# Kernel optimization log

Measured on AMD Instinct MI355X. Metric: run time of the kernel, lower is better.

Reference implementation:

```python
import jax, jax.numpy as jnp
import numpy as np

D_MODEL = 1024
N_HEADS = 16


def setup_inputs() -> dict:
    key = jax.random.key(0)
    ks = jax.random.split(key, 5)
    sigma = (1.0 / D_MODEL) ** 0.5
    return {
        "x": jax.random.normal(ks[0], (4, 2048, D_MODEL), dtype=jnp.float32),
        "W_q": jax.random.normal(ks[1], (D_MODEL, D_MODEL), dtype=jnp.float32) * sigma,
        "W_k": jax.random.normal(ks[2], (D_MODEL, D_MODEL), dtype=jnp.float32) * sigma,
        "W_v": jax.random.normal(ks[3], (D_MODEL, D_MODEL), dtype=jnp.float32) * sigma,
        "W_o": jax.random.normal(ks[4], (D_MODEL, D_MODEL), dtype=jnp.float32) * sigma,
    }


def reference(x, W_q, W_k, W_v, W_o):
    b, s, d = x.shape
    h = N_HEADS
    d_h = d // h
    # Projections: original does einsum('d_out dim, ... dim -> ... d_out') == x @ W.T
    def proj(W):
        y = jnp.einsum('bsd,ed->bse', x, W)
        # ... seq (head d_h) -> ... head seq d_h
        return y.reshape(b, s, h, d_h).transpose(0, 2, 1, 3)
    Q, K, V = proj(W_q), proj(W_k), proj(W_v)
    scale = 1.0 / jnp.sqrt(jnp.asarray(d_h, dtype=x.dtype))
    scores = jnp.einsum('bhqd,bhkd->bhqk', Q, K) * scale  # [b,h,s,s]
    causal = jnp.tril(jnp.ones((s, s), dtype=bool))
    scores = jnp.where(causal, scores, -jnp.inf)
    attn = jax.nn.softmax(scores, axis=-1)
    out = jnp.einsum('bhqk,bhkd->bhqd', attn, V)  # [b,h,s,d_h]
    out = out.transpose(0, 2, 1, 3).reshape(b, s, d)
    # einsum(Temp, W_o, '... dim1, dim dim1 -> ... dim') == Temp @ W_o.T
    return jnp.einsum('bse,de->bsd', out, W_o)
```

## Files before the change

kernel.cpp:

```cpp
#include <hip/hip_runtime.h>

typedef __attribute__((ext_vector_type(8))) short s16x8;
typedef __attribute__((ext_vector_type(4))) float f32x4;
typedef unsigned short u16;
typedef unsigned int u32;
typedef unsigned long long u64;

__device__ __forceinline__ u16 f2bf(float f) {
  unsigned u = __builtin_bit_cast(unsigned, f);
  return (u16)((u + 0x7fffu + ((u >> 16) & 1u)) >> 16);
}

#define QSCALE 0.18033688011112042f
#define MFIX 16.0f

__device__ __forceinline__ void gld16(const u16* g, u16* l) {
  __builtin_amdgcn_global_load_lds(
      (const __attribute__((address_space(1))) void*)g,
      (__attribute__((address_space(3))) void*)l, 16, 0, 0);
}

__device__ __forceinline__ u32 pack_trunc(float a, float b) {
  return __builtin_amdgcn_perm(__builtin_bit_cast(u32, b),
                               __builtin_bit_cast(u32, a), 0x07060302u);
}

__global__ __launch_bounds__(256)
void cvt_bf16(const float* __restrict__ src, u16* __restrict__ dst, int n8)
{
  const int i = blockIdx.x * 256 + threadIdx.x;
  if (i < n8) {
    f32x4 a = ((const f32x4*)src)[2 * i];
    f32x4 b = ((const f32x4*)src)[2 * i + 1];
    s16x8 pk;
    pk[0] = (short)f2bf(a[0]); pk[1] = (short)f2bf(a[1]);
    pk[2] = (short)f2bf(a[2]); pk[3] = (short)f2bf(a[3]);
    pk[4] = (short)f2bf(b[0]); pk[5] = (short)f2bf(b[1]);
    pk[6] = (short)f2bf(b[2]); pk[7] = (short)f2bf(b[3]);
    ((s16x8*)dst)[i] = pk;
  }
}

__global__ __launch_bounds__(256)
void cvt_bf16_w(const float* __restrict__ s0, const float* __restrict__ s1,
                const float* __restrict__ s2, const float* __restrict__ s3,
                u16* __restrict__ d0, u16* __restrict__ d1,
                u16* __restrict__ d2, u16* __restrict__ d3)
{
  const int ws = blockIdx.y;
  const float* src = (ws == 0) ? s0 : (ws == 1) ? s1 : (ws == 2) ? s2 : s3;
  u16* dst = (ws == 0) ? d0 : (ws == 1) ? d1 : (ws == 2) ? d2 : d3;
  const int i = blockIdx.x * 256 + threadIdx.x;
  f32x4 a = ((const f32x4*)src)[2 * i];
  f32x4 b = ((const f32x4*)src)[2 * i + 1];
  s16x8 pk;
  pk[0] = (short)f2bf(a[0]); pk[1] = (short)f2bf(a[1]);
  pk[2] = (short)f2bf(a[2]); pk[3] = (short)f2bf(a[3]);
  pk[4] = (short)f2bf(b[0]); pk[5] = (short)f2bf(b[1]);
  pk[6] = (short)f2bf(b[2]); pk[7] = (short)f2bf(b[3]);
  ((s16x8*)dst)[i] = pk;
}

__global__ __launch_bounds__(512)
void gemmQKV(const u16* __restrict__ A,
             const u16* __restrict__ B0, const u16* __restrict__ B1,
             const u16* __restrict__ B2,
             u16* __restrict__ o0, u16* __restrict__ o1, u16* __restrict__ o2)
{
  const int by = blockIdx.x;
  const int bx = blockIdx.y;
  const int bz = bx >> 2;
  const u16* Bw = (bz == 0) ? B0 : ((bz == 1) ? B1 : B2);
  u16* oQ = (bz == 0) ? o0 : ((bz == 1) ? o1 : o2);

  __shared__ u16 As[2][256 * 64];
  __shared__ u16 Bs[2][256 * 64];

  const int tid  = threadIdx.x;
  const int wid  = tid >> 6;
  const int lane = tid & 63;
  const int quad = lane >> 4;
  const int l15  = lane & 15;
  const int wr   = wid >> 2;
  const int wc   = wid & 3;

  const int srow = tid >> 3;
  const int scol = ((tid & 7) ^ (srow & 7)) * 8;
  const int wb8  = wid * 8;
  const u16* Ag = A  + (size_t)(by * 256) * 1024;
  const u16* Bg = Bw + (size_t)((bx & 3) * 256) * 1024;

#define STAGE(bf, kt)                                                          \
  do {                                                                         \
    _Pragma("unroll")                                                          \
    for (int c = 0; c < 4; ++c) {                                              \
      gld16(Ag + (size_t)(c * 64 + srow) * 1024 + (kt) * 64 + scol,            \
            &As[bf][(c * 64 + wb8) * 64]);                                     \
      gld16(Bg + (size_t)(c * 64 + srow) * 1024 + (kt) * 64 + scol,            \
            &Bs[bf][(c * 64 + wb8) * 64]);                                     \
    }                                                                          \
  } while (0)

  f32x4 acc[8][4];
  #pragma unroll
  for (int i = 0; i < 8; ++i)
    #pragma unroll
    for (int j = 0; j < 4; ++j)
      acc[i][j] = (f32x4){0.f, 0.f, 0.f, 0.f};

  const int swz = (l15 & 7) * 8;
  const int ca0 = (quad * 8) ^ swz;
  const int ca1 = (32 + quad * 8) ^ swz;

  STAGE(0, 0);
  STAGE(1, 1);
  asm volatile("s_waitcnt vmcnt(8)" ::: "memory");
  __builtin_amdgcn_s_barrier();
  __builtin_amdgcn_sched_barrier(0);

  for (int kt = 0; kt < 16; ++kt) {
    const int bf = kt & 1;
    const u16* Ab = &As[bf][(wr * 128) * 64];
    const u16* Bb = &Bs[bf][(wc * 64) * 64];
    __builtin_amdgcn_s_setprio(1);
    #pragma unroll
    for (int kh = 0; kh < 2; ++kh) {
      const int cc = kh ? ca1 : ca0;
      s16x8 bfr[4];
      #pragma unroll
      for (int nt = 0; nt < 4; ++nt)
        bfr[nt] = *(const s16x8*)&Bb[(nt * 16 + l15) * 64 + cc];
      #pragma unroll
      for (int mt = 0; mt < 8; ++mt) {
        s16x8 af = *(const s16x8*)&Ab[(mt * 16 + l15) * 64 + cc];
        #pragma unroll
        for (int nt = 0; nt < 4; ++nt)
          acc[mt][nt] = __builtin_amdgcn_mfma_f32_16x16x32_bf16(
              af, bfr[nt], acc[mt][nt], 0, 0, 0);
      }
    }
    __builtin_amdgcn_s_setprio(0);
    if (kt == 15) break;
    asm volatile("s_waitcnt lgkmcnt(0)" ::: "memory");
    __builtin_amdgcn_sched_barrier(0);
    __builtin_amdgcn_s_barrier();
    if (kt < 14) {
      STAGE(bf, kt + 2);
      asm volatile("s_waitcnt vmcnt(8)" ::: "memory");
    } else {
      asm volatile("s_waitcnt vmcnt(0)" ::: "memory");
    }
    __builtin_amdgcn_sched_barrier(0);
    __builtin_amdgcn_s_barrier();
    __builtin_amdgcn_sched_barrier(0);
  }

  #pragma unroll
  for (int mt = 0; mt < 8; ++mt)
    #pragma unroll
    for (int nt = 0; nt < 4; ++nt)
      #pragma unroll
      for (int r = 0; r < 4; ++r) {
        const int row = by * 256 + wr * 128 + mt * 16 + quad * 4 + r;
        const int col = (bx & 3) * 256 + wc * 64 + nt * 16 + l15;
        float v = acc[mt][nt][r];
        if (bz == 0) v *= QSCALE;
        const int b = row >> 11, s = row & 2047, hh = col >> 6, d = col & 63;
        oQ[(size_t)(b * 16 + hh) * 131072 + s * 64 + d] = f2bf(v);
      }
#undef STAGE
}

__global__ __launch_bounds__(256)
void gemm97o(const u16* __restrict__ A, const u16* __restrict__ B,
             float* __restrict__ oF)
{
  const int by = blockIdx.x;
  const int bx = blockIdx.y;

  __shared__ u16 As[128 * 32];
  __shared__ u16 Bs[128 * 32];

  const int tid  = threadIdx.x;
  const int w    = tid >> 6;
  const int lane = tid & 63;
  const int quad = lane >> 4;
  const int l15  = lane & 15;
  const int wm   = (w >> 1) * 64;
  const int wn   = (w & 1) * 64;

  const int arb  = w * 32;
  const int srow = lane >> 2;
  const int scol = (lane & 3) * 8;
  const u16* ga = A + (size_t)(by * 128 + arb + srow) * 1024 + scol;
  const u16* gb = B + (size_t)(bx * 128 + arb + srow) * 1024 + scol;
  u16* la0 = &As[arb * 32];
  u16* la1 = &As[(arb + 16) * 32];
  u16* lb0 = &Bs[arb * 32];
  u16* lb1 = &Bs[(arb + 16) * 32];

  f32x4 acc[4][4];
  #pragma unroll
  for (int i = 0; i < 4; ++i)
    #pragma unroll
    for (int j = 0; j < 4; ++j)
      acc[i][j] = (f32x4){0.f, 0.f, 0.f, 0.f};

  for (int k0 = 0; k0 < 1024; k0 += 32) {
    gld16(ga + k0,               la0);
    gld16(ga + k0 + 16 * 1024,   la1);
    gld16(gb + k0,               lb0);
    gld16(gb + k0 + 16 * 1024,   lb1);
    __syncthreads();

    s16x8 af[4], bf[4];
    #pragma unroll
    for (int i = 0; i < 4; ++i)
      af[i] = *(const s16x8*)&As[(wm + i * 16 + l15) * 32 + quad * 8];
    #pragma unroll
    for (int i = 0; i < 4; ++i)
      bf[i] = *(const s16x8*)&Bs[(wn + i * 16 + l15) * 32 + quad * 8];
    #pragma unroll
    for (int mt = 0; mt < 4; ++mt)
      #pragma unroll
      for (int nt = 0; nt < 4; ++nt)
        acc[mt][nt] = __builtin_amdgcn_mfma_f32_16x16x32_bf16(
            af[mt], bf[nt], acc[mt][nt], 0, 0, 0);
    __syncthreads();
  }

  #pragma unroll
  for (int mt = 0; mt < 4; ++mt)
    #pragma unroll
    for (int nt = 0; nt < 4; ++nt)
      #pragma unroll
      for (int r = 0; r < 4; ++r) {
        const int row = by * 128 + wm + mt * 16 + quad * 4 + r;
        const int col = bx * 128 + wn + nt * 16 + l15;
        oF[(size_t)row * 1024 + col] = acc[mt][nt][r];
      }
}

__global__ __launch_bounds__(256)
void vtrans(const u16* __restrict__ Vb, u16* __restrict__ VT)
{
  const int st = blockIdx.x;
  const int bh = blockIdx.y;
  __shared__ u16 T[64 * 72];
  const int tid = threadIdx.x;
  const size_t base = (size_t)bh * 131072;
  #pragma unroll
  for (int p = 0; p < 2; ++p) {
    const int idx = tid + p * 256;
    const int row = idx >> 3;
    const int col = (idx & 7) * 8;
    s16x8 v = *(const s16x8*)(Vb + base + (size_t)(st * 64 + row) * 64 + col);
    #pragma unroll
    for (int e = 0; e < 8; ++e) T[(col + e) * 72 + row] = v[e];
  }
  __syncthreads();
  #pragma unroll
  for (int p = 0; p < 2; ++p) {
    const int idx = tid + p * 256;
    const int drow = idx >> 3;
    const int scol = (idx & 7) * 8;
    *(s16x8*)(VT + base + (size_t)drow * 2048 + st * 64 + scol) =
        *(const s16x8*)&T[drow * 72 + scol];
  }
}

#define LOADKV(jj)                                                             \
  do {                                                                         \
    _Pragma("unroll")                                                          \
    for (int p = 0; p < 2; ++p) {                                              \
      const int idx = tid + p * 256;                                           \
      const int key = idx >> 3, col = (idx & 7) * 8;                           \
      kreg[p] = *(const s16x8*)(Kg + base + (size_t)((jj) * 64 + key) * 64 + col); \
    }                                                                          \
    _Pragma("unroll")                                                          \
    for (int p = 0; p < 2; ++p) {                                              \
      const int idx = tid + p * 256;                                           \
      const int d = idx >> 3, col = (idx & 7) * 8;                             \
      vreg[p] = *(const s16x8*)(VTg + base + (size_t)d * 2048 + (jj) * 64 + col); \
    }                                                                          \
  } while (0)

#define STOREKV()                                                              \
  do {                                                                         \
    _Pragma("unroll")                                                          \
    for (int p = 0; p < 2; ++p) {                                              \
      const int idx = tid + p * 256;                                           \
      const int key = idx >> 3, col = (idx & 7) * 8;                           \
      const int slot = (key & 3) * 16 + (key >> 2);                            \
      *(s16x8*)&Ks[slot * 72 + col] = kreg[p];                                 \
    }                                                                          \
    _Pragma("unroll")                                                          \
    for (int p = 0; p < 2; ++p) {                                              \
      const int idx = tid + p * 256;                                           \
      const int d = idx >> 3, col = (idx & 7) * 8;                             \
      *(s16x8*)&Vt[d * 72 + col] = vreg[p];                                    \
    }                                                                          \
  } while (0)

__global__ __launch_bounds__(256, 5)
void attn_kernel(const u16* __restrict__ Qg, const u16* __restrict__ Kg,
                 const u16* __restrict__ VTg, u16* __restrict__ out)
{
  const int bh = blockIdx.x;
  const int qt = 31 - blockIdx.y;
  const int b = bh >> 4, h = bh & 15;

  __shared__ u16 Ks[64 * 72];
  __shared__ u16 Vt[64 * 72];
  __shared__ u16 Ps[64 * 72];

  const int tid = threadIdx.x;
  const int w = tid >> 6, lane = tid & 63, quad = lane >> 4, l15 = lane & 15;
  const size_t base = (size_t)bh * 131072;

  s16x8 aq[2];
  #pragma unroll
  for (int ks = 0; ks < 2; ++ks)
    aq[ks] = *(const s16x8*)(Qg + base +
        (size_t)(qt * 64 + w * 16 + l15) * 64 + ks * 32 + quad * 8);

  u16* Pw = &Ps[(w * 16) * 72];

  s16x8 ones;
  #pragma unroll
  for (int e = 0; e < 8; ++e) ones[e] = (short)0x3F80;

  f32x4 O[4], liacc;
  #pragma unroll
  for (int dt = 0; dt < 4; ++dt) O[dt] = (f32x4){0.f, 0.f, 0.f, 0.f};
  liacc = (f32x4){0.f, 0.f, 0.f, 0.f};

  s16x8 kreg[2], vreg[2];
  LOADKV(0);
  STOREKV();
  __syncthreads();

  for (int j = 0; j <= qt; ++j) {
    if (j < qt) LOADKV(j + 1);

    f32x4 S[4];
    __builtin_amdgcn_s_setprio(1);
    #pragma unroll
    for (int nt = 0; nt < 4; ++nt) {
      s16x8 b0 = *(const s16x8*)&Ks[(nt * 16 + l15) * 72 + quad * 8];
      s16x8 b1 = *(const s16x8*)&Ks[(nt * 16 + l15) * 72 + 32 + quad * 8];
      f32x4 z = (f32x4){-MFIX, -MFIX, -MFIX, -MFIX};
      z = __builtin_amdgcn_mfma_f32_16x16x32_bf16(aq[0], b0, z, 0, 0, 0);
      z = __builtin_amdgcn_mfma_f32_16x16x32_bf16(aq[1], b1, z, 0, 0, 0);
      S[nt] = z;
    }
    __builtin_amdgcn_s_setprio(0);

    if (j == qt) {
      #pragma unroll
      for (int nt = 0; nt < 4; ++nt)
        #pragma unroll
        for (int r = 0; r < 4; ++r) {
          const int kg = 4 * l15 + nt;
          const int qg = w * 16 + quad * 4 + r;
          if (kg > qg) S[nt][r] = -1e30f;
        }
    }

    #pragma unroll
    for (int r = 0; r < 4; ++r) {
      const float p0 = __builtin_amdgcn_exp2f(S[0][r]);
      const float p1 = __builtin_amdgcn_exp2f(S[1][r]);
      const float p2 = __builtin_amdgcn_exp2f(S[2][r]);
      const float p3 = __builtin_amdgcn_exp2f(S[3][r]);
      const u64 pk = (u64)pack_trunc(p0, p1) |
                     ((u64)pack_trunc(p2, p3) << 32);
      *(u64*)&Pw[(quad * 4 + r) * 72 + 4 * l15] = pk;
    }
    s16x8 a0 = *(const s16x8*)&Pw[l15 * 72 + quad * 8];
    s16x8 a1 = *(const s16x8*)&Pw[l15 * 72 + 32 + quad * 8];

    __builtin_amdgcn_s_setprio(1);
    liacc = __builtin_amdgcn_mfma_f32_16x16x32_bf16(a0, ones, liacc, 0, 0, 0);
    liacc = __builtin_amdgcn_mfma_f32_16x16x32_bf16(a1, ones, liacc, 0, 0, 0);
    #pragma unroll
    for (int dt = 0; dt < 4; ++dt) {
      s16x8 b0 = *(const s16x8*)&Vt[(dt * 16 + l15) * 72 + quad * 8];
      s16x8 b1 = *(const s16x8*)&Vt[(dt * 16 + l15) * 72 + 32 + quad * 8];
      O[dt] = __builtin_amdgcn_mfma_f32_16x16x32_bf16(a0, b0, O[dt], 0, 0, 0);
      O[dt] = __builtin_amdgcn_mfma_f32_16x16x32_bf16(a1, b1, O[dt], 0, 0, 0);
    }
    __builtin_amdgcn_s_setprio(0);

    __syncthreads();
    if (j < qt) {
      STOREKV();
      __syncthreads();
    }
  }

  #pragma unroll
  for (int r = 0; r < 4; ++r) {
    const float inv = __builtin_amdgcn_rcpf(liacc[r]);
    const int sq = qt * 64 + w * 16 + quad * 4 + r;
    #pragma unroll
    for (int dt = 0; dt < 4; ++dt)
      out[(size_t)(b * 2048 + sq) * 1024 + h * 64 + dt * 16 + l15] =
          f2bf(O[dt][r] * inv);
  }
}

extern "C" void kernel_launch(void* const* d_in, const int* in_sizes, int n_in,
                              void* d_out, int out_size, void* d_ws, size_t ws_size,
                              hipStream_t stream) {
  (void)in_sizes; (void)n_in; (void)out_size; (void)ws_size;
  const float* x  = (const float*)d_in[0];
  const float* Wq = (const float*)d_in[1];
  const float* Wk = (const float*)d_in[2];
  const float* Wv = (const float*)d_in[3];
  const float* Wo = (const float*)d_in[4];
  float* out = (float*)d_out;

  u16* W16 = (u16*)d_ws;
  u16* xb  = W16;
  u16* VT  = W16;
  u16* Qb  = W16 + 8388608;
  u16* Kb  = W16 + 16777216;
  u16* Vb  = W16 + 25165824;
  u16* AO  = Vb;
  u16* Wqb = W16 + 33554432;
  u16* Wkb = Wqb + 1048576;
  u16* Wvb = Wkb + 1048576;
  u16* Wob = Wvb + 1048576;

  dim3 blk(256);
  cvt_bf16<<<dim3(4096), blk, 0, stream>>>(x,  xb,  1048576);
  cvt_bf16_w<<<dim3(512, 4), blk, 0, stream>>>(Wq, Wk, Wv, Wo,
                                               Wqb, Wkb, Wvb, Wob);

  gemmQKV<<<dim3(32, 12), dim3(512), 0, stream>>>(
      xb, Wqb, Wkb, Wvb, Qb, Kb, Vb);
  vtrans<<<dim3(32, 64), blk, 0, stream>>>(Vb, VT);
  attn_kernel<<<dim3(64, 32), blk, 0, stream>>>(Qb, Kb, VT, AO);
  gemm97o<<<dim3(64, 8), blk, 0, stream>>>(AO, Wob, out);
}
```

Before: 259.3 us.

## Fuse V transpose into QKV GEMM epilogue and halve N tile

The QKV projection GEMM now writes V directly in transposed [d, s] layout, so the separate vtrans kernel is dropped along with its extra read and write of V. The GEMM tile shrinks from 256x256 to 256x128 (grid doubles to 768 blocks) with a 4x2 wave layout, which reduces per-wave accumulators and LDS use. The workspace is remapped so the attention output reuses the xb region. The transposed V store is strided by 2048 elements per lane, so those writes are poorly coalesced, and the smaller tile lowers arithmetic intensity per block.

```diff
diff --git a/kernel.cpp b/kernel.cpp
--- a/kernel.cpp
+++ b/kernel.cpp
@@ -65,45 +65,46 @@
 void gemmQKV(const u16* __restrict__ A,
              const u16* __restrict__ B0, const u16* __restrict__ B1,
              const u16* __restrict__ B2,
-             u16* __restrict__ o0, u16* __restrict__ o1, u16* __restrict__ o2)
+             u16* __restrict__ o0, u16* __restrict__ o1, u16* __restrict__ oVT)
 {
   const int by = blockIdx.x;
   const int bx = blockIdx.y;
-  const int bz = bx >> 2;
+  const int bz = bx >> 3;
+  const int bn = bx & 7;
   const u16* Bw = (bz == 0) ? B0 : ((bz == 1) ? B1 : B2);
-  u16* oQ = (bz == 0) ? o0 : ((bz == 1) ? o1 : o2);
 
   __shared__ u16 As[2][256 * 64];
-  __shared__ u16 Bs[2][256 * 64];
+  __shared__ u16 Bs2[2][128 * 64];
 
   const int tid  = threadIdx.x;
   const int wid  = tid >> 6;
   const int lane = tid & 63;
   const int quad = lane >> 4;
   const int l15  = lane & 15;
-  const int wr   = wid >> 2;
-  const int wc   = wid & 3;
+  const int wr   = wid >> 1;
+  const int wc   = wid & 1;
 
   const int srow = tid >> 3;
   const int scol = ((tid & 7) ^ (srow & 7)) * 8;
   const int wb8  = wid * 8;
   const u16* Ag = A  + (size_t)(by * 256) * 1024;
-  const u16* Bg = Bw + (size_t)((bx & 3) * 256) * 1024;
+  const u16* Bg = Bw + (size_t)(bn * 128) * 1024;
 
 #define STAGE(bf, kt)                                                          \
   do {                                                                         \
     _Pragma("unroll")                                                          \
-    for (int c = 0; c < 4; ++c) {                                              \
+    for (int c = 0; c < 4; ++c)                                                \
       gld16(Ag + (size_t)(c * 64 + srow) * 1024 + (kt) * 64 + scol,            \
             &As[bf][(c * 64 + wb8) * 64]);                                     \
+    _Pragma("unroll")                                                          \
+    for (int c = 0; c < 2; ++c)                                                \
       gld16(Bg + (size_t)(c * 64 + srow) * 1024 + (kt) * 64 + scol,            \
-            &Bs[bf][(c * 64 + wb8) * 64]);                                     \
-    }                                                                          \
+            &Bs2[bf][(c * 64 + wb8) * 64]);                                    \
   } while (0)
 
-  f32x4 acc[8][4];
-  #pragma unroll
-  for (int i = 0; i < 8; ++i)
+  f32x4 acc[4][4];
+  #pragma unroll
+  for (int i = 0; i < 4; ++i)
     #pragma unroll
     for (int j = 0; j < 4; ++j)
       acc[i][j] = (f32x4){0.f, 0.f, 0.f, 0.f};
@@ -114,14 +115,14 @@
 
   STAGE(0, 0);
   STAGE(1, 1);
-  asm volatile("s_waitcnt vmcnt(8)" ::: "memory");
+  asm volatile("s_waitcnt vmcnt(6)" ::: "memory");
   __builtin_amdgcn_s_barrier();
   __builtin_amdgcn_sched_barrier(0);
 
   for (int kt = 0; kt < 16; ++kt) {
     const int bf = kt & 1;
-    const u16* Ab = &As[bf][(wr * 128) * 64];
-    const u16* Bb = &Bs[bf][(wc * 64) * 64];
+    const u16* Ab = &As[bf][(wr * 64) * 64];
+    const u16* Bb = &Bs2[bf][(wc * 64) * 64];
     __builtin_amdgcn_s_setprio(1);
     #pragma unroll
     for (int kh = 0; kh < 2; ++kh) {
@@ -131,7 +132,7 @@
       for (int nt = 0; nt < 4; ++nt)
         bfr[nt] = *(const s16x8*)&Bb[(nt * 16 + l15) * 64 + cc];
       #pragma unroll
-      for (int mt = 0; mt < 8; ++mt) {
+      for (int mt = 0; mt < 4; ++mt) {
         s16x8 af = *(const s16x8*)&Ab[(mt * 16 + l15) * 64 + cc];
         #pragma unroll
         for (int nt = 0; nt < 4; ++nt)
@@ -146,7 +147,7 @@
     __builtin_amdgcn_s_barrier();
     if (kt < 14) {
       STAGE(bf, kt + 2);
-      asm volatile("s_waitcnt vmcnt(8)" ::: "memory");
+      asm volatile("s_waitcnt vmcnt(6)" ::: "memory");
     } else {
       asm volatile("s_waitcnt vmcnt(0)" ::: "memory");
     }
@@ -156,17 +157,23 @@
   }
 
   #pragma unroll
-  for (int mt = 0; mt < 8; ++mt)
+  for (int mt = 0; mt < 4; ++mt)
     #pragma unroll
     for (int nt = 0; nt < 4; ++nt)
       #pragma unroll
       for (int r = 0; r < 4; ++r) {
-        const int row = by * 256 + wr * 128 + mt * 16 + quad * 4 + r;
-        const int col = (bx & 3) * 256 + wc * 64 + nt * 16 + l15;
+        const int row = by * 256 + wr * 64 + mt * 16 + quad * 4 + r;
+        const int colw = bn * 128 + wc * 64 + nt * 16 + l15;
         float v = acc[mt][nt][r];
-        if (bz == 0) v *= QSCALE;
-        const int b = row >> 11, s = row & 2047, hh = col >> 6, d = col & 63;
-        oQ[(size_t)(b * 16 + hh) * 131072 + s * 64 + d] = f2bf(v);
+        const int b = row >> 11, s = row & 2047;
+        const int hh = colw >> 6, d = colw & 63;
+        if (bz == 0) {
+          o0[(size_t)(b * 16 + hh) * 131072 + s * 64 + d] = f2bf(v * QSCALE);
+        } else if (bz == 1) {
+          o1[(size_t)(b * 16 + hh) * 131072 + s * 64 + d] = f2bf(v);
+        } else {
+          oVT[(size_t)(b * 16 + hh) * 131072 + (size_t)d * 2048 + s] = f2bf(v);
+        }
       }
 #undef STAGE
 }
@@ -239,34 +246,6 @@
         const int col = bx * 128 + wn + nt * 16 + l15;
         oF[(size_t)row * 1024 + col] = acc[mt][nt][r];
       }
-}
-
-__global__ __launch_bounds__(256)
-void vtrans(const u16* __restrict__ Vb, u16* __restrict__ VT)
-{
-  const int st = blockIdx.x;
-  const int bh = blockIdx.y;
-  __shared__ u16 T[64 * 72];
-  const int tid = threadIdx.x;
-  const size_t base = (size_t)bh * 131072;
-  #pragma unroll
-  for (int p = 0; p < 2; ++p) {
-    const int idx = tid + p * 256;
-    const int row = idx >> 3;
-    const int col = (idx & 7) * 8;
-    s16x8 v = *(const s16x8*)(Vb + base + (size_t)(st * 64 + row) * 64 + col);
-    #pragma unroll
-    for (int e = 0; e < 8; ++e) T[(col + e) * 72 + row] = v[e];
-  }
-  __syncthreads();
-  #pragma unroll
-  for (int p = 0; p < 2; ++p) {
-    const int idx = tid + p * 256;
-    const int drow = idx >> 3;
-    const int scol = (idx & 7) * 8;
-    *(s16x8*)(VT + base + (size_t)drow * 2048 + st * 64 + scol) =
-        *(const s16x8*)&T[drow * 72 + scol];
-  }
 }
 
 #define LOADKV(jj)                                                             \
@@ -423,11 +402,10 @@
 
   u16* W16 = (u16*)d_ws;
   u16* xb  = W16;
-  u16* VT  = W16;
+  u16* AO  = W16;
   u16* Qb  = W16 + 8388608;
   u16* Kb  = W16 + 16777216;
-  u16* Vb  = W16 + 25165824;
-  u16* AO  = Vb;
+  u16* VT  = W16 + 25165824;
   u16* Wqb = W16 + 33554432;
   u16* Wkb = Wqb + 1048576;
   u16* Wvb = Wkb + 1048576;
@@ -438,9 +416,8 @@
   cvt_bf16_w<<<dim3(512, 4), blk, 0, stream>>>(Wq, Wk, Wv, Wo,
                                                Wqb, Wkb, Wvb, Wob);
 
-  gemmQKV<<<dim3(32, 12), dim3(512), 0, stream>>>(
-      xb, Wqb, Wkb, Wvb, Qb, Kb, Vb);
-  vtrans<<<dim3(32, 64), blk, 0, stream>>>(Vb, VT);
+  gemmQKV<<<dim3(32, 24), dim3(512), 0, stream>>>(
+      xb, Wqb, Wkb, Wvb, Qb, Kb, VT);
   attn_kernel<<<dim3(64, 32), blk, 0, stream>>>(Qb, Kb, VT, AO);
   gemm97o<<<dim3(64, 8), blk, 0, stream>>>(AO, Wob, out);
 }
```

Result: slower. 264.5 us (+2.0%).

## Fuse V transpose into a separate V projection GEMM epilogue

Applied to the files above, without the earlier changes.

Splits the fused QKV projection into a QK kernel plus a V kernel. The V kernel reuses the smaller 128x128 GEMM and writes V directly in transposed [b,h,d,s] layout, which removes the standalone vtrans kernel and its extra read/write of V. In exchange, V is computed by a less tuned GEMM without double buffering, the scattered transposed stores are uncoalesced (consecutive lanes write addresses 2048 elements apart), and there is one more launch boundary. The workspace aliasing is also reorganised so AO shares the xb buffer.

```diff
diff --git a/kernel.cpp b/kernel.cpp
--- a/kernel.cpp
+++ b/kernel.cpp
@@ -62,16 +62,16 @@
 }
 
 __global__ __launch_bounds__(512)
-void gemmQKV(const u16* __restrict__ A,
-             const u16* __restrict__ B0, const u16* __restrict__ B1,
-             const u16* __restrict__ B2,
-             u16* __restrict__ o0, u16* __restrict__ o1, u16* __restrict__ o2)
+void gemmQK(const u16* __restrict__ A,
+            const u16* __restrict__ B0, const u16* __restrict__ B1,
+            u16* __restrict__ o0, u16* __restrict__ o1)
 {
   const int by = blockIdx.x;
   const int bx = blockIdx.y;
   const int bz = bx >> 2;
-  const u16* Bw = (bz == 0) ? B0 : ((bz == 1) ? B1 : B2);
-  u16* oQ = (bz == 0) ? o0 : ((bz == 1) ? o1 : o2);
+  const int bn = bx & 3;
+  const u16* Bw = (bz == 0) ? B0 : B1;
+  u16* oQ = (bz == 0) ? o0 : o1;
 
   __shared__ u16 As[2][256 * 64];
   __shared__ u16 Bs[2][256 * 64];
@@ -88,7 +88,7 @@
   const int scol = ((tid & 7) ^ (srow & 7)) * 8;
   const int wb8  = wid * 8;
   const u16* Ag = A  + (size_t)(by * 256) * 1024;
-  const u16* Bg = Bw + (size_t)((bx & 3) * 256) * 1024;
+  const u16* Bg = Bw + (size_t)(bn * 256) * 1024;
 
 #define STAGE(bf, kt)                                                          \
   do {                                                                         \
@@ -162,18 +162,18 @@
       #pragma unroll
       for (int r = 0; r < 4; ++r) {
         const int row = by * 256 + wr * 128 + mt * 16 + quad * 4 + r;
-        const int col = (bx & 3) * 256 + wc * 64 + nt * 16 + l15;
+        const int col = bn * 256 + wc * 64 + nt * 16 + l15;
         float v = acc[mt][nt][r];
+        const int b = row >> 11, s = row & 2047, hh = col >> 6, d = col & 63;
         if (bz == 0) v *= QSCALE;
-        const int b = row >> 11, s = row & 2047, hh = col >> 6, d = col & 63;
         oQ[(size_t)(b * 16 + hh) * 131072 + s * 64 + d] = f2bf(v);
       }
 #undef STAGE
 }
 
 __global__ __launch_bounds__(256)
-void gemm97o(const u16* __restrict__ A, const u16* __restrict__ B,
-             float* __restrict__ oF)
+void gemmV(const u16* __restrict__ A, const u16* __restrict__ B,
+           u16* __restrict__ oVT)
 {
   const int by = blockIdx.x;
   const int bx = blockIdx.y;
@@ -237,36 +237,80 @@
       for (int r = 0; r < 4; ++r) {
         const int row = by * 128 + wm + mt * 16 + quad * 4 + r;
         const int col = bx * 128 + wn + nt * 16 + l15;
+        const int b = row >> 11, s = row & 2047, hh = col >> 6, d = col & 63;
+        oVT[(size_t)(b * 16 + hh) * 131072 + (size_t)d * 2048 + s] =
+            f2bf(acc[mt][nt][r]);
+      }
+}
+
+__global__ __launch_bounds__(256)
+void gemm97o(const u16* __restrict__ A, const u16* __restrict__ B,
+             float* __restrict__ oF)
+{
+  const int by = blockIdx.x;
+  const int bx = blockIdx.y;
+
+  __shared__ u16 As[128 * 32];
+  __shared__ u16 Bs[128 * 32];
+
+  const int tid  = threadIdx.x;
+  const int w    = tid >> 6;
+  const int lane = tid & 63;
+  const int quad = lane >> 4;
+  const int l15  = lane & 15;
+  const int wm   = (w >> 1) * 64;
+  const int wn   = (w & 1) * 64;
+
+  const int arb  = w * 32;
+  const int srow = lane >> 2;
+  const int scol = (lane & 3) * 8;
+  const u16* ga = A + (size_t)(by * 128 + arb + srow) * 1024 + scol;
+  const u16* gb = B + (size_t)(bx * 128 + arb + srow) * 1024 + scol;
+  u16* la0 = &As[arb * 32];
+  u16* la1 = &As[(arb + 16) * 32];
+  u16* lb0 = &Bs[arb * 32];
+  u16* lb1 = &Bs[(arb + 16) * 32];
+
+  f32x4 acc[4][4];
+  #pragma unroll
+  for (int i = 0; i < 4; ++i)
+    #pragma unroll
+    for (int j = 0; j < 4; ++j)
+      acc[i][j] = (f32x4){0.f, 0.f, 0.f, 0.f};
+
+  for (int k0 = 0; k0 < 1024; k0 += 32) {
+    gld16(ga + k0,               la0);
+    gld16(ga + k0 + 16 * 1024,   la1);
+    gld16(gb + k0,               lb0);
+    gld16(gb + k0 + 16 * 1024,   lb1);
+    __syncthreads();
+
+    s16x8 af[4], bf[4];
+    #pragma unroll
+    for (int i = 0; i < 4; ++i)
+      af[i] = *(const s16x8*)&As[(wm + i * 16 + l15) * 32 + quad * 8];
+    #pragma unroll
+    for (int i = 0; i < 4; ++i)
+      bf[i] = *(const s16x8*)&Bs[(wn + i * 16 + l15) * 32 + quad * 8];
+    #pragma unroll
+    for (int mt = 0; mt < 4; ++mt)
+      #pragma unroll
+      for (int nt = 0; nt < 4; ++nt)
+        acc[mt][nt] = __builtin_amdgcn_mfma_f32_16x16x32_bf16(
+            af[mt], bf[nt], acc[mt][nt], 0, 0, 0);
+    __syncthreads();
+  }
+
+  #pragma unroll
+  for (int mt = 0; mt < 4; ++mt)
+    #pragma unroll
+    for (int nt = 0; nt < 4; ++nt)
+      #pragma unroll
+      for (int r = 0; r < 4; ++r) {
+        const int row = by * 128 + wm + mt * 16 + quad * 4 + r;
+        const int col = bx * 128 + wn + nt * 16 + l15;
         oF[(size_t)row * 1024 + col] = acc[mt][nt][r];
       }
-}
-
-__global__ __launch_bounds__(256)
-void vtrans(const u16* __restrict__ Vb, u16* __restrict__ VT)
-{
-  const int st = blockIdx.x;
-  const int bh = blockIdx.y;
-  __shared__ u16 T[64 * 72];
-  const int tid = threadIdx.x;
-  const size_t base = (size_t)bh * 131072;
-  #pragma unroll
-  for (int p = 0; p < 2; ++p) {
-    const int idx = tid + p * 256;
-    const int row = idx >> 3;
-    const int col = (idx & 7) * 8;
-    s16x8 v = *(const s16x8*)(Vb + base + (size_t)(st * 64 + row) * 64 + col);
-    #pragma unroll
-    for (int e = 0; e < 8; ++e) T[(col + e) * 72 + row] = v[e];
-  }
-  __syncthreads();
-  #pragma unroll
-  for (int p = 0; p < 2; ++p) {
-    const int idx = tid + p * 256;
-    const int drow = idx >> 3;
-    const int scol = (idx & 7) * 8;
-    *(s16x8*)(VT + base + (size_t)drow * 2048 + st * 64 + scol) =
-        *(const s16x8*)&T[drow * 72 + scol];
-  }
 }
 
 #define LOADKV(jj)                                                             \
@@ -423,11 +467,10 @@
 
   u16* W16 = (u16*)d_ws;
   u16* xb  = W16;
-  u16* VT  = W16;
+  u16* AO  = W16;
   u16* Qb  = W16 + 8388608;
   u16* Kb  = W16 + 16777216;
-  u16* Vb  = W16 + 25165824;
-  u16* AO  = Vb;
+  u16* VT  = W16 + 25165824;
   u16* Wqb = W16 + 33554432;
   u16* Wkb = Wqb + 1048576;
   u16* Wvb = Wkb + 1048576;
@@ -438,9 +481,8 @@
   cvt_bf16_w<<<dim3(512, 4), blk, 0, stream>>>(Wq, Wk, Wv, Wo,
                                                Wqb, Wkb, Wvb, Wob);
 
-  gemmQKV<<<dim3(32, 12), dim3(512), 0, stream>>>(
-      xb, Wqb, Wkb, Wvb, Qb, Kb, Vb);
-  vtrans<<<dim3(32, 64), blk, 0, stream>>>(Vb, VT);
+  gemmQK<<<dim3(32, 8), dim3(512), 0, stream>>>(xb, Wqb, Wkb, Qb, Kb);
+  gemmV<<<dim3(64, 8), blk, 0, stream>>>(xb, Wvb, VT);
   attn_kernel<<<dim3(64, 32), blk, 0, stream>>>(Qb, Kb, VT, AO);
   gemm97o<<<dim3(64, 8), blk, 0, stream>>>(AO, Wob, out);
 }
```

Measured after the change: 246.9 us. 1.05x faster.
